# Performance work log

Measured on AMD Instinct MI355X. Metric: run time of the kernel, lower is better.

Reference implementation:

```python
import jax, jax.numpy as jnp
import numpy as np

B, C, N, K, O = 8, 64, 4096, 16, 64  # batch, in_channels, nodes, knn, out_channels


def setup_inputs() -> dict:
    key = jax.random.key(0)
    k1, k2, k3 = jax.random.split(key, 3)
    x = jax.random.normal(k1, (B, C, N, 1), dtype=jnp.float32)
    # edge_index[0] = source (neighbor) idx, edge_index[1] = target (center) idx
    src = jax.random.randint(k2, (B, N, K), 0, N, dtype=jnp.int32)
    dst = jnp.broadcast_to(jnp.arange(N, dtype=jnp.int32)[None, :, None], (B, N, K))
    edge_index = jnp.stack([src, dst], axis=0)  # [2, B, N, K]
    # BasicLayer([2C, O]) == Linear(2C, O, bias=True) + ReLU (norm=None)
    W = jax.random.normal(k3, (2 * C, O), dtype=jnp.float32) * (1.0 / np.sqrt(2 * C))
    b = jnp.zeros((O,), dtype=jnp.float32)
    return {"x": x, "edge_index": edge_index, "W": W, "b": b}


def reference(x, edge_index, W, b):
    Bs, Cs, Ns, _ = x.shape
    # [B, C, N, 1] -> [B*N, C] node feature matrix
    xf = x.squeeze(-1).transpose(0, 2, 1).reshape(Bs * Ns, Cs)
    # convert per-batch indices to global node ids (offset by b*N), flatten edges
    off = (jnp.arange(Bs, dtype=edge_index.dtype) * Ns)[None, :, None, None]
    ei = (edge_index + off).reshape(2, -1)  # [2, E]
    src, dst = ei[0], ei[1]
    x_i = xf[dst]          # target/center features  [E, C]
    x_j = xf[src]          # source/neighbor features [E, C]
    # EdgeConv message: MLP(concat(x_i, x_j - x_i))
    h = jax.nn.relu(jnp.concatenate([x_i, x_j - x_i], axis=-1) @ W + b)  # [E, O]
    # max-aggregate messages onto target nodes
    out = jax.ops.segment_max(h, dst, num_segments=Bs * Ns)  # [B*N, O]
    Os = out.shape[-1]
    return out.reshape(Bs, Ns, Os).transpose(0, 2, 1)[..., None]  # [B, O, N, 1]
```

## Files before the change

### kernel.cpp

```cpp
#include <hip/hip_runtime.h>
#include <hip/hip_bf16.h>


#define BB 8
#define CC 64
#define NN 4096
#define KK 16
#define OO 64

typedef __bf16 bf16x8 __attribute__((ext_vector_type(8)));
typedef float f32x4 __attribute__((ext_vector_type(4)));

union Frag { int4 i; bf16x8 v; };
union PackA { bf16x8 v; __hip_bfloat16 h[8]; };

__global__ __launch_bounds__(256, 3) void g_gemm(
    const float* __restrict__ x, const float* __restrict__ W,
    __hip_bfloat16* __restrict__ G) {
    __shared__ float xt[64][65];
    __shared__ int4 wfl[8][64];

    int t = threadIdx.x, w = t >> 6, l = t & 63;
    int b = blockIdx.x >> 6;
    int n0 = (blockIdx.x & 63) << 6;

    const float* xb = x + (size_t)b * CC * NN;
    #pragma unroll
    for (int it = 0; it < 4; ++it) {
        int idx = it * 256 + t, c = idx >> 4, q = idx & 15;
        float4 v = *(const float4*)(xb + (size_t)c * NN + n0 + q * 4);
        xt[c][q * 4 + 0] = v.x; xt[c][q * 4 + 1] = v.y;
        xt[c][q * 4 + 2] = v.z; xt[c][q * 4 + 3] = v.w;
    }
    {
        __hip_bfloat16* wlu = (__hip_bfloat16*)wfl;
        int o = t & 63, h = t >> 6;
        #pragma unroll
        for (int kk = 0; kk < 16; ++kk) {
            int k = h * 16 + kk;
            float wb = W[(64 + k) * OO + o];
            int gq = (k >> 3) & 3, j = k & 7, ks = k >> 5;
            int lane = (gq << 4) | (o & 15);
            int fs = ks * 4 + (o >> 4);
            wlu[((fs * 64 + lane) << 3) | j] = __float2bfloat16(wb);
        }
    }
    __syncthreads();

    Frag wf[2][4];
    #pragma unroll
    for (int ks = 0; ks < 2; ++ks)
        #pragma unroll
        for (int ot = 0; ot < 4; ++ot)
            wf[ks][ot].i = wfl[ks * 4 + ot][l];

    f32x4 acc[4];
    #pragma unroll
    for (int ot = 0; ot < 4; ++ot) acc[ot] = f32x4{0.f, 0.f, 0.f, 0.f};

    int node = (w << 4) + (l & 15);
    #pragma unroll
    for (int ks = 0; ks < 2; ++ks) {
        PackA a;
        #pragma unroll
        for (int j = 0; j < 8; ++j)
            a.h[j] = __float2bfloat16(xt[ks * 32 + ((l >> 4) << 3) + j][node]);
        #pragma unroll
        for (int ot = 0; ot < 4; ++ot)
            acc[ot] = __builtin_amdgcn_mfma_f32_16x16x32_bf16(a.v, wf[ks][ot].v, acc[ot], 0, 0, 0);
    }

    size_t base = ((size_t)b * NN + n0 + (w << 4)) * 64;
    #pragma unroll
    for (int ot = 0; ot < 4; ++ot)
        #pragma unroll
        for (int r = 0; r < 4; ++r) {
            int nd = ((l >> 4) << 2) + r;
            G[base + (size_t)nd * 64 + ot * 16 + (l & 15)] = __float2bfloat16(acc[ot][r]);
        }
}

__global__ __launch_bounds__(256, 4) void gather_max(
    const float* __restrict__ x, const int* __restrict__ ei,
    const float* __restrict__ W, const float* __restrict__ bias,
    const uint2* __restrict__ Gq, float* __restrict__ out) {
    __shared__ union { float xt[64][33]; float ot_[64][33]; } sm;
    __shared__ int4 wfl[8][64];
    __shared__ float Fl[32][65];

    int t = threadIdx.x, w = t >> 6, l = t & 63;
    int b = blockIdx.x >> 7;
    int n0 = (blockIdx.x & 127) << 5;

    const float* xb = x + (size_t)b * CC * NN;
    #pragma unroll
    for (int it = 0; it < 8; ++it) {
        int idx = it * 256 + t, c = idx >> 5, nn = idx & 31;
        sm.xt[c][nn] = xb[(size_t)c * NN + n0 + nn];
    }
    {
        __hip_bfloat16* wlu = (__hip_bfloat16*)wfl;
        int o = t & 63, h = t >> 6;
        #pragma unroll
        for (int kk = 0; kk < 16; ++kk) {
            int k = h * 16 + kk;
            float v = W[k * OO + o] - W[(64 + k) * OO + o];
            int gq = (k >> 3) & 3, j = k & 7, ks = k >> 5;
            int lane = (gq << 4) | (o & 15);
            int fs = ks * 4 + (o >> 4);
            wlu[((fs * 64 + lane) << 3) | j] = __float2bfloat16(v);
        }
    }
    const int* srcp = ei + (size_t)b * NN * KK;
    int nb = n0 + (w << 3);
    int eg = l >> 4, c = l & 15;
    int idxv[8];
    #pragma unroll
    for (int i = 0; i < 8; ++i) idxv[i] = srcp[(nb + i) * KK + c];
    __syncthreads();

    {
        int ng = (w & 1) << 4;
        int ob = (w >> 1) << 1;
        Frag wfA[2][2];
        #pragma unroll
        for (int ks = 0; ks < 2; ++ks)
            #pragma unroll
            for (int oo = 0; oo < 2; ++oo)
                wfA[ks][oo].i = wfl[ks * 4 + ob + oo][l];
        f32x4 acc[2];
        #pragma unroll
        for (int oo = 0; oo < 2; ++oo) {
            float bv = bias[(ob + oo) * 16 + (l & 15)];
            acc[oo] = f32x4{bv, bv, bv, bv};
        }
        #pragma unroll
        for (int ks = 0; ks < 2; ++ks) {
            PackA a;
            #pragma unroll
            for (int j = 0; j < 8; ++j)
                a.h[j] = __float2bfloat16(sm.xt[ks * 32 + ((l >> 4) << 3) + j][ng + (l & 15)]);
            #pragma unroll
            for (int oo = 0; oo < 2; ++oo)
                acc[oo] = __builtin_amdgcn_mfma_f32_16x16x32_bf16(a.v, wfA[ks][oo].v, acc[oo], 0, 0, 0);
        }
        #pragma unroll
        for (int oo = 0; oo < 2; ++oo)
            #pragma unroll
            for (int r = 0; r < 4; ++r)
                Fl[ng + ((l >> 4) << 2) + r][(ob + oo) * 16 + (l & 15)] = acc[oo][r];
    }
    __syncthreads();

    size_t bbase = (size_t)b * NN;
    uint2 g[8][4];
    #pragma unroll
    for (int i = 0; i < 8; ++i)
        #pragma unroll
        for (int q = 0; q < 4; ++q) {
            int vk = __shfl(idxv[i], (q << 2) | eg);
            g[i][q] = Gq[((size_t)bbase + vk) * 16 + c];
        }

    #pragma unroll
    for (int i = 0; i < 8; ++i) {
        float m0 = -3.4e38f, m1 = -3.4e38f, m2 = -3.4e38f, m3 = -3.4e38f;
        #pragma unroll
        for (int q = 0; q < 4; ++q) {
            m0 = fmaxf(m0, __uint_as_float(g[i][q].x << 16));
            m1 = fmaxf(m1, __uint_as_float(g[i][q].x & 0xffff0000u));
            m2 = fmaxf(m2, __uint_as_float(g[i][q].y << 16));
            m3 = fmaxf(m3, __uint_as_float(g[i][q].y & 0xffff0000u));
        }
        m0 = fmaxf(m0, __shfl_xor(m0, 16)); m0 = fmaxf(m0, __shfl_xor(m0, 32));
        m1 = fmaxf(m1, __shfl_xor(m1, 16)); m1 = fmaxf(m1, __shfl_xor(m1, 32));
        m2 = fmaxf(m2, __shfl_xor(m2, 16)); m2 = fmaxf(m2, __shfl_xor(m2, 32));
        m3 = fmaxf(m3, __shfl_xor(m3, 16)); m3 = fmaxf(m3, __shfl_xor(m3, 32));
        if (eg == (i & 3)) {
            int nl = (w << 3) + i;
            sm.ot_[4 * c + 0][nl] = fmaxf(Fl[nl][4 * c + 0] + m0, 0.0f);
            sm.ot_[4 * c + 1][nl] = fmaxf(Fl[nl][4 * c + 1] + m1, 0.0f);
            sm.ot_[4 * c + 2][nl] = fmaxf(Fl[nl][4 * c + 2] + m2, 0.0f);
            sm.ot_[4 * c + 3][nl] = fmaxf(Fl[nl][4 * c + 3] + m3, 0.0f);
        }
    }
    __syncthreads();

    float* ob2 = out + (size_t)b * OO * NN;
    #pragma unroll
    for (int it = 0; it < 8; ++it) {
        int idx = it * 256 + t, o = idx >> 5, nn = idx & 31;
        ob2[(size_t)o * NN + n0 + nn] = sm.ot_[o][nn];
    }
}

extern "C" void kernel_launch(void* const* d_in, const int* in_sizes, int n_in,
                              void* d_out, int out_size, void* d_ws, size_t ws_size,
                              hipStream_t stream) {
    const float* x    = (const float*)d_in[0];
    const int*   ei   = (const int*)d_in[1];
    const float* W    = (const float*)d_in[2];
    const float* bias = (const float*)d_in[3];
    float* out = (float*)d_out;

    __hip_bfloat16* G = (__hip_bfloat16*)d_ws;

    hipLaunchKernelGGL(g_gemm, dim3(BB * (NN / 64)), dim3(256), 0, stream, x, W, G);
    hipLaunchKernelGGL(gather_max, dim3(BB * (NN / 32)), dim3(256), 0, stream,
                       x, ei, W, bias, (const uint2*)G, out);
}
```

Baseline: 24.41 us.

## Bind each batch to one XCD via hardware XCC id and atomic tile counters

Both kernels now read the hardware XCC id and use it as the batch index, so every workgroup running on a given chiplet processes only that batch's tiles. Tiles are handed out through per-batch atomic counters in the workspace, which are zeroed with a memset before launch. The aim is to keep each batch's G table and x data resident in a single XCD's L2, so the random neighbor gathers hit locally. In exchange it adds an atomic plus a barrier per tile and a memset launch, and it assumes exactly eight XCDs with round-robin dispatch, relying on the counters for correctness when block placement is uneven.

```diff
diff --git a/kernel.cpp b/kernel.cpp
--- a/kernel.cpp
+++ b/kernel.cpp
@@ -14,24 +14,20 @@
 union Frag { int4 i; bf16x8 v; };
 union PackA { bf16x8 v; __hip_bfloat16 h[8]; };
 
-__global__ __launch_bounds__(256, 3) void g_gemm(
+static constexpr size_t G_BYTES = (size_t)BB * NN * 64 * 2;
+
+__global__ __launch_bounds__(256, 3) void g_gemm_xcd(
     const float* __restrict__ x, const float* __restrict__ W,
-    __hip_bfloat16* __restrict__ G) {
+    __hip_bfloat16* __restrict__ G, unsigned* __restrict__ ctr) {
     __shared__ float xt[64][65];
     __shared__ int4 wfl[8][64];
+    __shared__ unsigned s_t;
 
     int t = threadIdx.x, w = t >> 6, l = t & 63;
-    int b = blockIdx.x >> 6;
-    int n0 = (blockIdx.x & 63) << 6;
-
-    const float* xb = x + (size_t)b * CC * NN;
-    #pragma unroll
-    for (int it = 0; it < 4; ++it) {
-        int idx = it * 256 + t, c = idx >> 4, q = idx & 15;
-        float4 v = *(const float4*)(xb + (size_t)c * NN + n0 + q * 4);
-        xt[c][q * 4 + 0] = v.x; xt[c][q * 4 + 1] = v.y;
-        xt[c][q * 4 + 2] = v.z; xt[c][q * 4 + 3] = v.w;
-    }
+    unsigned xreg;
+    asm volatile("s_getreg_b32 %0, hwreg(HW_REG_XCC_ID)" : "=s"(xreg));
+    int b = (int)(xreg & 7);
+
     {
         __hip_bfloat16* wlu = (__hip_bfloat16*)wfl;
         int o = t & 63, h = t >> 6;
@@ -46,7 +42,6 @@
         }
     }
     __syncthreads();
-
     Frag wf[2][4];
     #pragma unroll
     for (int ks = 0; ks < 2; ++ks)
@@ -54,50 +49,64 @@
         for (int ot = 0; ot < 4; ++ot)
             wf[ks][ot].i = wfl[ks * 4 + ot][l];
 
-    f32x4 acc[4];
-    #pragma unroll
-    for (int ot = 0; ot < 4; ++ot) acc[ot] = f32x4{0.f, 0.f, 0.f, 0.f};
-
+    const float* xb = x + (size_t)b * CC * NN;
     int node = (w << 4) + (l & 15);
-    #pragma unroll
-    for (int ks = 0; ks < 2; ++ks) {
-        PackA a;
-        #pragma unroll
-        for (int j = 0; j < 8; ++j)
-            a.h[j] = __float2bfloat16(xt[ks * 32 + ((l >> 4) << 3) + j][node]);
+
+    for (;;) {
+        if (t == 0) s_t = atomicAdd(&ctr[b], 1u);
+        __syncthreads();
+        unsigned tt = s_t;
+        if (tt >= 64u) break;
+        int n0 = (int)tt << 6;
+
+        #pragma unroll
+        for (int it = 0; it < 4; ++it) {
+            int idx = it * 256 + t, c = idx >> 4, q = idx & 15;
+            float4 v = *(const float4*)(xb + (size_t)c * NN + n0 + q * 4);
+            xt[c][q * 4 + 0] = v.x; xt[c][q * 4 + 1] = v.y;
+            xt[c][q * 4 + 2] = v.z; xt[c][q * 4 + 3] = v.w;
+        }
+        __syncthreads();
+
+        f32x4 acc[4];
+        #pragma unroll
+        for (int ot = 0; ot < 4; ++ot) acc[ot] = f32x4{0.f, 0.f, 0.f, 0.f};
+        #pragma unroll
+        for (int ks = 0; ks < 2; ++ks) {
+            PackA a;
+            #pragma unroll
+            for (int j = 0; j < 8; ++j)
+                a.h[j] = __float2bfloat16(xt[ks * 32 + ((l >> 4) << 3) + j][node]);
+            #pragma unroll
+            for (int ot = 0; ot < 4; ++ot)
+                acc[ot] = __builtin_amdgcn_mfma_f32_16x16x32_bf16(a.v, wf[ks][ot].v, acc[ot], 0, 0, 0);
+        }
+        size_t base = ((size_t)b * NN + n0 + (w << 4)) * 64;
         #pragma unroll
         for (int ot = 0; ot < 4; ++ot)
-            acc[ot] = __builtin_amdgcn_mfma_f32_16x16x32_bf16(a.v, wf[ks][ot].v, acc[ot], 0, 0, 0);
-    }
-
-    size_t base = ((size_t)b * NN + n0 + (w << 4)) * 64;
-    #pragma unroll
-    for (int ot = 0; ot < 4; ++ot)
-        #pragma unroll
-        for (int r = 0; r < 4; ++r) {
-            int nd = ((l >> 4) << 2) + r;
-            G[base + (size_t)nd * 64 + ot * 16 + (l & 15)] = __float2bfloat16(acc[ot][r]);
-        }
+            #pragma unroll
+            for (int r = 0; r < 4; ++r) {
+                int nd = ((l >> 4) << 2) + r;
+                G[base + (size_t)nd * 64 + ot * 16 + (l & 15)] = __float2bfloat16(acc[ot][r]);
+            }
+    }
 }
 
-__global__ __launch_bounds__(256, 4) void gather_max(
+__global__ __launch_bounds__(256, 4) void gather_max_xcd(
     const float* __restrict__ x, const int* __restrict__ ei,
     const float* __restrict__ W, const float* __restrict__ bias,
-    const uint2* __restrict__ Gq, float* __restrict__ out) {
+    const uint2* __restrict__ Gq, float* __restrict__ out,
+    unsigned* __restrict__ ctr) {
     __shared__ union { float xt[64][33]; float ot_[64][33]; } sm;
     __shared__ int4 wfl[8][64];
     __shared__ float Fl[32][65];
+    __shared__ unsigned s_t;
 
     int t = threadIdx.x, w = t >> 6, l = t & 63;
-    int b = blockIdx.x >> 7;
-    int n0 = (blockIdx.x & 127) << 5;
-
-    const float* xb = x + (size_t)b * CC * NN;
-    #pragma unroll
-    for (int it = 0; it < 8; ++it) {
-        int idx = it * 256 + t, c = idx >> 5, nn = idx & 31;
-        sm.xt[c][nn] = xb[(size_t)c * NN + n0 + nn];
-    }
+    unsigned xreg;
+    asm volatile("s_getreg_b32 %0, hwreg(HW_REG_XCC_ID)" : "=s"(xreg));
+    int b = (int)(xreg & 7);
+
     {
         __hip_bfloat16* wlu = (__hip_bfloat16*)wfl;
         int o = t & 63, h = t >> 6;
@@ -111,86 +120,103 @@
             wlu[((fs * 64 + lane) << 3) | j] = __float2bfloat16(v);
         }
     }
+    __syncthreads();
+
+    int ng = (w & 1) << 4, ob = (w >> 1) << 1;
+    Frag wfA[2][2];
+    #pragma unroll
+    for (int ks = 0; ks < 2; ++ks)
+        #pragma unroll
+        for (int oo = 0; oo < 2; ++oo)
+            wfA[ks][oo].i = wfl[ks * 4 + ob + oo][l];
+    float bv[2];
+    #pragma unroll
+    for (int oo = 0; oo < 2; ++oo) bv[oo] = bias[(ob + oo) * 16 + (l & 15)];
+
+    const float* xb = x + (size_t)b * CC * NN;
     const int* srcp = ei + (size_t)b * NN * KK;
-    int nb = n0 + (w << 3);
+    size_t bbase = (size_t)b * NN;
+    float* ob2 = out + (size_t)b * OO * NN;
     int eg = l >> 4, c = l & 15;
-    int idxv[8];
-    #pragma unroll
-    for (int i = 0; i < 8; ++i) idxv[i] = srcp[(nb + i) * KK + c];
-    __syncthreads();
-
-    {
-        int ng = (w & 1) << 4;
-        int ob = (w >> 1) << 1;
-        Frag wfA[2][2];
-        #pragma unroll
-        for (int ks = 0; ks < 2; ++ks)
+
+    for (;;) {
+        if (t == 0) s_t = atomicAdd(&ctr[8 + b], 1u);
+        __syncthreads();
+        unsigned tt = s_t;
+        if (tt >= 128u) break;
+        int n0 = (int)tt << 5;
+        int nb = n0 + (w << 3);
+
+        #pragma unroll
+        for (int it = 0; it < 8; ++it) {
+            int idx = it * 256 + t, cc2 = idx >> 5, nn = idx & 31;
+            sm.xt[cc2][nn] = xb[(size_t)cc2 * NN + n0 + nn];
+        }
+        int idxv[8];
+        #pragma unroll
+        for (int i = 0; i < 8; ++i) idxv[i] = srcp[(nb + i) * KK + c];
+        __syncthreads();
+
+        {
+            f32x4 acc[2];
+            #pragma unroll
+            for (int oo = 0; oo < 2; ++oo) acc[oo] = f32x4{bv[oo], bv[oo], bv[oo], bv[oo]};
+            #pragma unroll
+            for (int ks = 0; ks < 2; ++ks) {
+                PackA a;
+                #pragma unroll
+                for (int j = 0; j < 8; ++j)
+                    a.h[j] = __float2bfloat16(sm.xt[ks * 32 + ((l >> 4) << 3) + j][ng + (l & 15)]);
+                #pragma unroll
+                for (int oo = 0; oo < 2; ++oo)
+                    acc[oo] = __builtin_amdgcn_mfma_f32_16x16x32_bf16(a.v, wfA[ks][oo].v, acc[oo], 0, 0, 0);
+            }
             #pragma unroll
             for (int oo = 0; oo < 2; ++oo)
-                wfA[ks][oo].i = wfl[ks * 4 + ob + oo][l];
-        f32x4 acc[2];
-        #pragma unroll
-        for (int oo = 0; oo < 2; ++oo) {
-            float bv = bias[(ob + oo) * 16 + (l & 15)];
-            acc[oo] = f32x4{bv, bv, bv, bv};
-        }
-        #pragma unroll
-        for (int ks = 0; ks < 2; ++ks) {
-            PackA a;
-            #pragma unroll
-            for (int j = 0; j < 8; ++j)
-                a.h[j] = __float2bfloat16(sm.xt[ks * 32 + ((l >> 4) << 3) + j][ng + (l & 15)]);
-            #pragma unroll
-            for (int oo = 0; oo < 2; ++oo)
-                acc[oo] = __builtin_amdgcn_mfma_f32_16x16x32_bf16(a.v, wfA[ks][oo].v, acc[oo], 0, 0, 0);
-        }
-        #pragma unroll
-        for (int oo = 0; oo < 2; ++oo)
-            #pragma unroll
-            for (int r = 0; r < 4; ++r)
-                Fl[ng + ((l >> 4) << 2) + r][(ob + oo) * 16 + (l & 15)] = acc[oo][r];
-    }
-    __syncthreads();
-
-    size_t bbase = (size_t)b * NN;
-    uint2 g[8][4];
-    #pragma unroll
-    for (int i = 0; i < 8; ++i)
-        #pragma unroll
-        for (int q = 0; q < 4; ++q) {
-            int vk = __shfl(idxv[i], (q << 2) | eg);
-            g[i][q] = Gq[((size_t)bbase + vk) * 16 + c];
-        }
-
-    #pragma unroll
-    for (int i = 0; i < 8; ++i) {
-        float m0 = -3.4e38f, m1 = -3.4e38f, m2 = -3.4e38f, m3 = -3.4e38f;
-        #pragma unroll
-        for (int q = 0; q < 4; ++q) {
-            m0 = fmaxf(m0, __uint_as_float(g[i][q].x << 16));
-            m1 = fmaxf(m1, __uint_as_float(g[i][q].x & 0xffff0000u));
-            m2 = fmaxf(m2, __uint_as_float(g[i][q].y << 16));
-            m3 = fmaxf(m3, __uint_as_float(g[i][q].y & 0xffff0000u));
-        }
-        m0 = fmaxf(m0, __shfl_xor(m0, 16)); m0 = fmaxf(m0, __shfl_xor(m0, 32));
-        m1 = fmaxf(m1, __shfl_xor(m1, 16)); m1 = fmaxf(m1, __shfl_xor(m1, 32));
-        m2 = fmaxf(m2, __shfl_xor(m2, 16)); m2 = fmaxf(m2, __shfl_xor(m2, 32));
-        m3 = fmaxf(m3, __shfl_xor(m3, 16)); m3 = fmaxf(m3, __shfl_xor(m3, 32));
-        if (eg == (i & 3)) {
-            int nl = (w << 3) + i;
-            sm.ot_[4 * c + 0][nl] = fmaxf(Fl[nl][4 * c + 0] + m0, 0.0f);
-            sm.ot_[4 * c + 1][nl] = fmaxf(Fl[nl][4 * c + 1] + m1, 0.0f);
-            sm.ot_[4 * c + 2][nl] = fmaxf(Fl[nl][4 * c + 2] + m2, 0.0f);
-            sm.ot_[4 * c + 3][nl] = fmaxf(Fl[nl][4 * c + 3] + m3, 0.0f);
-        }
-    }
-    __syncthreads();
-
-    float* ob2 = out + (size_t)b * OO * NN;
-    #pragma unroll
-    for (int it = 0; it < 8; ++it) {
-        int idx = it * 256 + t, o = idx >> 5, nn = idx & 31;
-        ob2[(size_t)o * NN + n0 + nn] = sm.ot_[o][nn];
+                #pragma unroll
+                for (int r = 0; r < 4; ++r)
+                    Fl[ng + ((l >> 4) << 2) + r][(ob + oo) * 16 + (l & 15)] = acc[oo][r];
+        }
+        __syncthreads();
+
+        uint2 g[8][4];
+        #pragma unroll
+        for (int i = 0; i < 8; ++i)
+            #pragma unroll
+            for (int q = 0; q < 4; ++q) {
+                int vk = __shfl(idxv[i], (q << 2) | eg);
+                g[i][q] = Gq[(bbase + (size_t)vk) * 16 + c];
+            }
+
+        #pragma unroll
+        for (int i = 0; i < 8; ++i) {
+            float m0 = -3.4e38f, m1 = -3.4e38f, m2 = -3.4e38f, m3 = -3.4e38f;
+            #pragma unroll
+            for (int q = 0; q < 4; ++q) {
+                m0 = fmaxf(m0, __uint_as_float(g[i][q].x << 16));
+                m1 = fmaxf(m1, __uint_as_float(g[i][q].x & 0xffff0000u));
+                m2 = fmaxf(m2, __uint_as_float(g[i][q].y << 16));
+                m3 = fmaxf(m3, __uint_as_float(g[i][q].y & 0xffff0000u));
+            }
+            m0 = fmaxf(m0, __shfl_xor(m0, 16)); m0 = fmaxf(m0, __shfl_xor(m0, 32));
+            m1 = fmaxf(m1, __shfl_xor(m1, 16)); m1 = fmaxf(m1, __shfl_xor(m1, 32));
+            m2 = fmaxf(m2, __shfl_xor(m2, 16)); m2 = fmaxf(m2, __shfl_xor(m2, 32));
+            m3 = fmaxf(m3, __shfl_xor(m3, 16)); m3 = fmaxf(m3, __shfl_xor(m3, 32));
+            if (eg == (i & 3)) {
+                int nl = (w << 3) + i;
+                sm.ot_[4 * c + 0][nl] = fmaxf(Fl[nl][4 * c + 0] + m0, 0.0f);
+                sm.ot_[4 * c + 1][nl] = fmaxf(Fl[nl][4 * c + 1] + m1, 0.0f);
+                sm.ot_[4 * c + 2][nl] = fmaxf(Fl[nl][4 * c + 2] + m2, 0.0f);
+                sm.ot_[4 * c + 3][nl] = fmaxf(Fl[nl][4 * c + 3] + m3, 0.0f);
+            }
+        }
+        __syncthreads();
+
+        #pragma unroll
+        for (int it = 0; it < 8; ++it) {
+            int idx = it * 256 + t, o = idx >> 5, nn = idx & 31;
+            ob2[(size_t)o * NN + n0 + nn] = sm.ot_[o][nn];
+        }
     }
 }
 
@@ -204,8 +230,10 @@
     float* out = (float*)d_out;
 
     __hip_bfloat16* G = (__hip_bfloat16*)d_ws;
-
-    hipLaunchKernelGGL(g_gemm, dim3(BB * (NN / 64)), dim3(256), 0, stream, x, W, G);
-    hipLaunchKernelGGL(gather_max, dim3(BB * (NN / 32)), dim3(256), 0, stream,
-                       x, ei, W, bias, (const uint2*)G, out);
+    unsigned* ctr = (unsigned*)((char*)d_ws + G_BYTES);
+
+    hipMemsetAsync(ctr, 0, 128, stream);
+    hipLaunchKernelGGL(g_gemm_xcd, dim3(512), dim3(256), 0, stream, x, W, G, ctr);
+    hipLaunchKernelGGL(gather_max_xcd, dim3(1024), dim3(256), 0, stream,
+                       x, ei, W, bias, (const uint2*)G, out, ctr);
 }
```

New measurement: 52.04 us. 2.13x slower.
